# Performance work log

Hardware: AMD Instinct MI355X
Metric: run time of the kernel (lower is better)

Reference implementation:

```python
import jax, jax.numpy as jnp
import numpy as np

B, C, H, W = 4, 64, 64, 64
C2 = 2 * C
CR = C2 // 16  # SE bottleneck

def setup_inputs() -> dict:
    key = jax.random.key(0)
    ks = jax.random.split(key, 8)
    stdv = 1.0 / np.sqrt(C)
    return {
        "x1": jax.random.normal(ks[0], (B, C, H, W), jnp.float32),
        "x2": jax.random.normal(ks[1], (B, C, H, W), jnp.float32),
        "weight": jax.random.uniform(ks[2], (C, C), jnp.float32, -stdv, stdv),
        "weight2": jax.random.uniform(ks[3], (C, C), jnp.float32, -stdv, stdv),
        "ca_fc1": jax.random.normal(ks[4], (CR, C2), jnp.float32) * 0.05,  # 1x1 conv as matrix
        "ca_fc2": jax.random.normal(ks[5], (C2, CR), jnp.float32) * 0.05,
        "conv_w": jax.random.normal(ks[6], (C, C2), jnp.float32) * 0.05,  # 1x1 conv 2C->C
        "conv_b": jnp.zeros((C,), jnp.float32),
    }

def reference(x1, x2, weight, weight2, ca_fc1, ca_fc2, conv_w, conv_b):
    b, c, h, w = x2.shape
    n = h * w
    a1 = x1.reshape(b, c, n)  # x1 flattened [B,C,N]
    a2 = x2.reshape(b, c, n)  # x2 flattened [B,C,N]
    # Non-local branch: f = theta_x @ phi_x = a1^T @ a2 -> [B,N,N]
    f = jnp.einsum('bcn,bcm->bnm', a1, a2)
    adj = jax.nn.softmax(f, axis=-1)
    support = jnp.einsum('bcn,cd->bnd', a2, weight)  # g_x @ W, [B,N,C]
    y = jnp.einsum('bnm,bmd->bnd', adj, support)     # adj @ support
    y = y.transpose(0, 2, 1).reshape(b, c, h, w)
    # Channel-affinity branch: c_x = a_x @ b_x -> [B,C,C]
    c_x = jnp.einsum('bcn,bdn->bcd', a1, a2)
    support2 = jnp.einsum('bcd,de->bce', c_x, weight2)   # [B,C,C]
    y2 = jnp.einsum('bcd,bdn->bcn', support2, a1).reshape(b, c, h, w)
    z = jnp.concatenate([y, y2], axis=1)  # [B,2C,H,W]
    # ChannelAttention: global max pool -> fc1 -> relu -> fc2 -> sigmoid
    mp = jnp.max(z, axis=(2, 3))                       # [B,2C]
    hdn = jax.nn.relu(jnp.einsum('be,re->br', mp, ca_fc1))
    v = jax.nn.sigmoid(jnp.einsum('br,er->be', hdn, ca_fc2))  # [B,2C]
    out = z * v[:, :, None, None] + z
    out = jnp.einsum('behw,oe->bohw', out, conv_w) + conv_b[None, :, None, None]
    return out
```

## Files before the change

### kernel.cpp

```cpp
#include <hip/hip_runtime.h>
#include <hip/hip_bf16.h>
#include <math.h>

#define B_   4
#define C_   64
#define N_   4096
#define C2_  128

using frag  = __attribute__((ext_vector_type(8))) short;
using f32x4 = __attribute__((ext_vector_type(4))) float;
using f4    = __attribute__((ext_vector_type(4))) float;

__device__ __forceinline__ unsigned short f2bf(float f) {
  unsigned int u = __float_as_uint(f);
  u += 0x7fffu + ((u >> 16) & 1u);
  return (unsigned short)(u >> 16);
}
__device__ __forceinline__ float bf2f(unsigned short h) {
  return __uint_as_float(((unsigned int)h) << 16);
}
__device__ __forceinline__ unsigned int pkbf(float a, float b) {
  __hip_bfloat16 ha = __float2bfloat16(a), hb = __float2bfloat16(b);
  unsigned short ua, ub;
  __builtin_memcpy(&ua, &ha, 2);
  __builtin_memcpy(&ub, &hb, 2);
  return (unsigned int)ua | ((unsigned int)ub << 16);
}
__device__ __forceinline__ frag pk8(f4 lo, f4 hi) {
  frag f;
  unsigned int* u = (unsigned int*)&f;
  u[0] = pkbf(lo.x, lo.y);
  u[1] = pkbf(lo.z, lo.w);
  u[2] = pkbf(hi.x, hi.y);
  u[3] = pkbf(hi.z, hi.w);
  return f;
}
__device__ __forceinline__ f4 max4(f4 a, f4 b) {
  return (f4){fmaxf(a.x, b.x), fmaxf(a.y, b.y), fmaxf(a.z, b.z), fmaxf(a.w, b.w)};
}

__global__ __launch_bounds__(256) void prep_kernel(const float* __restrict__ x1,
                                                   const float* __restrict__ x2,
                                                   unsigned short* __restrict__ a1t,
                                                   unsigned short* __restrict__ a2t) {
  __shared__ float tA[64 * 33];
  __shared__ float tB[64 * 33];
  int b = blockIdx.y, n0 = blockIdx.x * 32, tid = threadIdx.x;
  {
    int n = tid & 31, cq = tid >> 5;
#pragma unroll
    for (int k = 0; k < 8; ++k) {
      int c = cq + 8 * k;
      tA[c * 33 + n] = x2[((size_t)(b * C_ + c)) * N_ + n0 + n];
      tB[c * 33 + n] = x1[((size_t)(b * C_ + c)) * N_ + n0 + n];
    }
  }
  __syncthreads();
  {
    int c = tid & 63, nq = tid >> 6;
#pragma unroll
    for (int k = 0; k < 8; ++k) {
      int n2 = nq + 4 * k;
      a2t[((size_t)b * N_ + n0 + n2) * C_ + c] = f2bf(tA[c * 33 + n2]);
      a1t[((size_t)b * N_ + n0 + n2) * C_ + c] = f2bf(tB[c * 33 + n2]);
    }
  }
}

__global__ __launch_bounds__(256) void support_mm_kernel(const float* __restrict__ weight,
                                                         const unsigned short* __restrict__ a2t,
                                                         unsigned short* __restrict__ vT) {
  __shared__ float Wl[64 * 65];
  int b = blockIdx.y, n0 = blockIdx.x * 32, tid = threadIdx.x;
  int wave = tid >> 6, lane = tid & 63, l16 = lane & 15, lq = lane >> 4;
#pragma unroll
  for (int k = 0; k < 16; ++k) {
    int lin = tid + 256 * k;
    Wl[(lin >> 6) * 65 + (lin & 63)] = weight[lin];
  }
  frag b0[2], b1[2];
#pragma unroll
  for (int ng = 0; ng < 2; ++ng) {
    const unsigned short* bp = a2t + ((size_t)b * N_ + n0 + ng * 16 + l16) * C_;
    b0[ng] = *(const frag*)(bp + lq * 8);
    b1[ng] = *(const frag*)(bp + 32 + lq * 8);
  }
  __syncthreads();
  int dd = 16 * wave + l16;
  frag aw[2];
#pragma unroll
  for (int ks = 0; ks < 2; ++ks) {
    float wv[8];
#pragma unroll
    for (int j = 0; j < 8; ++j) wv[j] = Wl[(ks * 32 + lq * 8 + j) * 65 + dd];
    aw[ks] = pk8((f4){wv[0], wv[1], wv[2], wv[3]}, (f4){wv[4], wv[5], wv[6], wv[7]});
  }
  f32x4 acc[2];
#pragma unroll
  for (int ng = 0; ng < 2; ++ng) {
    acc[ng] = (f32x4){0.f, 0.f, 0.f, 0.f};
    acc[ng] = __builtin_amdgcn_mfma_f32_16x16x32_bf16(aw[0], b0[ng], acc[ng], 0, 0, 0);
    acc[ng] = __builtin_amdgcn_mfma_f32_16x16x32_bf16(aw[1], b1[ng], acc[ng], 0, 0, 0);
  }
#pragma unroll
  for (int ng = 0; ng < 2; ++ng)
#pragma unroll
    for (int r = 0; r < 4; ++r)
      vT[((size_t)(b * C_) + 16 * wave + 4 * lq + r) * N_ + n0 + ng * 16 + l16] =
          f2bf(acc[ng][r]);
}

__global__ __launch_bounds__(256) void cxmm_kernel(const float* __restrict__ x1,
                                                   const float* __restrict__ x2,
                                                   float* __restrict__ cxp) {
  int b = blockIdx.y, seg = blockIdx.x, tid = threadIdx.x;
  int wave = tid >> 6, lane = tid & 63, l16 = lane & 15, lq = lane >> 4;
  int n0 = seg * 64;
  const float* a2r = x2 + ((size_t)(b * C_) + 16 * wave + l16) * N_ + n0 + lq * 8;
  frag afr[2];
#pragma unroll
  for (int ks = 0; ks < 2; ++ks)
    afr[ks] = pk8(*(const f4*)(a2r + ks * 32), *(const f4*)(a2r + ks * 32 + 4));
  f32x4 acc[4];
#pragma unroll
  for (int cg = 0; cg < 4; ++cg) acc[cg] = (f32x4){0.f, 0.f, 0.f, 0.f};
#pragma unroll
  for (int cg = 0; cg < 4; ++cg) {
    const float* a1r = x1 + ((size_t)(b * C_) + cg * 16 + l16) * N_ + n0 + lq * 8;
#pragma unroll
    for (int ks = 0; ks < 2; ++ks) {
      frag bfr = pk8(*(const f4*)(a1r + ks * 32), *(const f4*)(a1r + ks * 32 + 4));
      acc[cg] = __builtin_amdgcn_mfma_f32_16x16x32_bf16(afr[ks], bfr, acc[cg], 0, 0, 0);
    }
  }
  float* op = cxp + ((size_t)(b * 64 + seg)) * 4096;
#pragma unroll
  for (int cg = 0; cg < 4; ++cg)
#pragma unroll
    for (int r = 0; r < 4; ++r)
      op[(16 * wave + 4 * lq + r) * 64 + cg * 16 + l16] = acc[cg][r];
}

__global__ __launch_bounds__(256) void cxred_kernel(const float* __restrict__ cxp,
                                                    float* __restrict__ cx) {
  int idx = blockIdx.x * 256 + threadIdx.x;
  int b = idx >> 12, r = idx & 4095;
  const float* p = cxp + (size_t)b * 64 * 4096 + r;
  float s = 0.f;
#pragma unroll 8
  for (int sg = 0; sg < 64; ++sg) s += p[(size_t)sg * 4096];
  cx[idx] = s;
}

__global__ __launch_bounds__(256) void s2bf_kernel(const float* __restrict__ cx,
                                                   const float* __restrict__ w2,
                                                   unsigned short* __restrict__ s2bf) {
  __shared__ float cxl[4096];
  __shared__ float w2l[4096];
  int b = blockIdx.x, tid = threadIdx.x;
#pragma unroll
  for (int k = 0; k < 16; ++k) {
    int lin = tid + 256 * k;
    cxl[lin] = cx[(size_t)b * 4096 + lin];
    w2l[lin] = w2[lin];
  }
  __syncthreads();
  int c = tid & 63, eg = tid >> 6;
  float acc[16];
#pragma unroll
  for (int i = 0; i < 16; ++i) acc[i] = 0.f;
  for (int d = 0; d < 64; ++d) {
    float a = cxl[d * 64 + c];
#pragma unroll
    for (int i = 0; i < 16; ++i) acc[i] += a * w2l[d * 64 + eg * 16 + i];
  }
  unsigned short* op = s2bf + (size_t)b * 4096 + c * 64 + eg * 16;
#pragma unroll
  for (int i = 0; i < 8; ++i)
    *(unsigned int*)(op + 2 * i) = pkbf(acc[2 * i], acc[2 * i + 1]);
}

template <int SEG>
__global__ __launch_bounds__(256) void attn_kernel(const unsigned short* __restrict__ a1t,
                                                   const unsigned short* __restrict__ a2t,
                                                   const unsigned short* __restrict__ vT,
                                                   float* __restrict__ z,
                                                   unsigned short* __restrict__ Opart,
                                                   float* __restrict__ ml) {
  __shared__ unsigned short Kt[2][64 * 64];
  __shared__ unsigned short Vt[2][64 * 64];
  __shared__ uint2 Pl[4][16 * 16];

  const int b = blockIdx.y, n0 = blockIdx.x * 64, tid = threadIdx.x;
  const int seg = (SEG > 1) ? blockIdx.z : 0;
  const int wave = tid >> 6, lane = tid & 63;
  const int l16 = lane & 15, lq = lane >> 4;
  const int NT = N_ / SEG / 64;
  const int mbase = seg * (N_ / SEG);

  const unsigned short* qbase = a1t + ((size_t)b * N_ + n0 + wave * 16 + l16) * C_;
  frag qa0 = *(const frag*)(qbase + lq * 8);
  frag qa1 = *(const frag*)(qbase + 32 + lq * 8);

  f32x4 O[4];
#pragma unroll
  for (int i = 0; i < 4; ++i) O[i] = (f32x4){0.f, 0.f, 0.f, 0.f};
  float m_l = -1e30f, l_l = 0.f;

  const unsigned short* a2b = a2t + (size_t)b * N_ * C_;
  const unsigned short* vTb = vT + (size_t)b * C_ * N_;
  char* Pw = (char*)&Pl[wave][0];
  const int swzP = (l16 & 7) << 4;

  const int srow0 = tid >> 3, scb = tid & 7;
  const int srow1 = (tid + 256) >> 3;
  const int kswz0 = (scb * 16) ^ ((srow0 & 7) << 4);
  const int kswz1 = (scb * 16) ^ ((srow1 & 7) << 4);

  frag k0 = *(const frag*)(a2b + (size_t)(mbase + srow0) * C_ + scb * 8);
  frag k1 = *(const frag*)(a2b + (size_t)(mbase + srow1) * C_ + scb * 8);
  frag v0 = *(const frag*)(vTb + (size_t)srow0 * N_ + mbase + scb * 8);
  frag v1 = *(const frag*)(vTb + (size_t)srow1 * N_ + mbase + scb * 8);
  *(frag*)((char*)&Kt[0][0] + srow0 * 128 + kswz0) = k0;
  *(frag*)((char*)&Kt[0][0] + srow1 * 128 + kswz1) = k1;
  *(frag*)((char*)&Vt[0][0] + srow0 * 128 + kswz0) = v0;
  *(frag*)((char*)&Vt[0][0] + srow1 * 128 + kswz1) = v1;
  __syncthreads();

  int cur = 0;
  for (int t = 0; t < NT; ++t, cur ^= 1) {
    if (t + 1 < NT) {
      int mn = mbase + (t + 1) * 64;
      k0 = *(const frag*)(a2b + (size_t)(mn + srow0) * C_ + scb * 8);
      k1 = *(const frag*)(a2b + (size_t)(mn + srow1) * C_ + scb * 8);
      v0 = *(const frag*)(vTb + (size_t)srow0 * N_ + mn + scb * 8);
      v1 = *(const frag*)(vTb + (size_t)srow1 * N_ + mn + scb * 8);
    }

    f32x4 S[4];
    __builtin_amdgcn_s_setprio(1);
#pragma unroll
    for (int ms = 0; ms < 4; ++ms) {
      int m = ms * 16 + l16;
      int swz = (m & 7) << 4;
      frag kb0 = *(const frag*)((char*)&Kt[cur][0] + m * 128 + ((lq * 16) ^ swz));
      frag kb1 = *(const frag*)((char*)&Kt[cur][0] + m * 128 + ((64 + lq * 16) ^ swz));
      f32x4 acc = (f32x4){0.f, 0.f, 0.f, 0.f};
      acc = __builtin_amdgcn_mfma_f32_16x16x32_bf16(kb0, qa0, acc, 0, 0, 0);
      acc = __builtin_amdgcn_mfma_f32_16x16x32_bf16(kb1, qa1, acc, 0, 0, 0);
      S[ms] = acc;
    }
    __builtin_amdgcn_s_setprio(0);

    float mx0 = fmaxf(fmaxf(S[0][0], S[0][1]), fmaxf(S[0][2], S[0][3]));
    float mx1 = fmaxf(fmaxf(S[1][0], S[1][1]), fmaxf(S[1][2], S[1][3]));
    float mx2 = fmaxf(fmaxf(S[2][0], S[2][1]), fmaxf(S[2][2], S[2][3]));
    float mx3 = fmaxf(fmaxf(S[3][0], S[3][1]), fmaxf(S[3][2], S[3][3]));
    float mx = fmaxf(fmaxf(mx0, mx1), fmaxf(mx2, mx3));
    mx = fmaxf(mx, __shfl_xor(mx, 16, 64));
    mx = fmaxf(mx, __shfl_xor(mx, 32, 64));

    if (!__all(mx <= m_l + 8.f)) {
      float mn = fmaxf(m_l, mx);
      float sc = __expf(m_l - mn);
      m_l = mn;
      l_l *= sc;
      float scb_[4];
#pragma unroll
      for (int r = 0; r < 4; ++r) scb_[r] = __shfl(sc, 20 * lq + r, 64);
#pragma unroll
      for (int ds = 0; ds < 4; ++ds)
#pragma unroll
        for (int r = 0; r < 4; ++r) O[ds][r] *= scb_[r];
    }

    float p[16];
    float rs = 0.f;
#pragma unroll
    for (int ms = 0; ms < 4; ++ms)
#pragma unroll
      for (int r = 0; r < 4; ++r) {
        float e = __expf(S[ms][r] - m_l);
        p[ms * 4 + r] = e;
        rs += e;
      }
    rs += __shfl_xor(rs, 16, 64);
    rs += __shfl_xor(rs, 32, 64);
    l_l += rs;

#pragma unroll
    for (int ms = 0; ms < 4; ++ms) {
      uint2 w;
      w.x = pkbf(p[ms * 4 + 0], p[ms * 4 + 1]);
      w.y = pkbf(p[ms * 4 + 2], p[ms * 4 + 3]);
      *(uint2*)(Pw + l16 * 128 + ((32 * ms + 8 * lq) ^ swzP)) = w;
    }
    asm volatile("s_waitcnt lgkmcnt(0)" ::: "memory");
    __builtin_amdgcn_sched_barrier(0);

    frag pa0 = *(const frag*)(Pw + l16 * 128 + ((lq * 16) ^ swzP));
    frag pa1 = *(const frag*)(Pw + l16 * 128 + ((64 + lq * 16) ^ swzP));
    __builtin_amdgcn_s_setprio(1);
#pragma unroll
    for (int ds = 0; ds < 4; ++ds) {
      int d = ds * 16 + l16;
      int swz = (d & 7) << 4;
      frag vb0 = *(const frag*)((char*)&Vt[cur][0] + d * 128 + ((lq * 16) ^ swz));
      frag vb1 = *(const frag*)((char*)&Vt[cur][0] + d * 128 + ((64 + lq * 16) ^ swz));
      O[ds] = __builtin_amdgcn_mfma_f32_16x16x32_bf16(pa0, vb0, O[ds], 0, 0, 0);
      O[ds] = __builtin_amdgcn_mfma_f32_16x16x32_bf16(pa1, vb1, O[ds], 0, 0, 0);
    }
    __builtin_amdgcn_s_setprio(0);

    if (t + 1 < NT) {
      *(frag*)((char*)&Kt[cur ^ 1][0] + srow0 * 128 + kswz0) = k0;
      *(frag*)((char*)&Kt[cur ^ 1][0] + srow1 * 128 + kswz1) = k1;
      *(frag*)((char*)&Vt[cur ^ 1][0] + srow0 * 128 + kswz0) = v0;
      *(frag*)((char*)&Vt[cur ^ 1][0] + srow1 * 128 + kswz1) = v1;
      __syncthreads();
    }
  }

  if (SEG > 1) {
    size_t base = (size_t)(b * SEG + seg) * N_ + n0 + wave * 16;
    if (lq == 0) {
      ml[(base + l16) * 2]     = m_l;
      ml[(base + l16) * 2 + 1] = l_l;
    }
#pragma unroll
    for (int r = 0; r < 4; ++r)
#pragma unroll
      for (int ds = 0; ds < 4; ++ds)
        Opart[(base + lq * 4 + r) * 64 + ds * 16 + l16] = f2bf(O[ds][r]);
  } else {
    float inv[4];
#pragma unroll
    for (int r = 0; r < 4; ++r) inv[r] = 1.f / __shfl(l_l, 20 * lq + r, 64);
#pragma unroll
    for (int ds = 0; ds < 4; ++ds)
#pragma unroll
      for (int r = 0; r < 4; ++r)
        z[((size_t)b * N_ + n0 + wave * 16 + lq * 4 + r) * 128 + ds * 16 + l16] = O[ds][r] * inv[r];
  }
}

__global__ __launch_bounds__(256) void combine_kernel(const unsigned short* __restrict__ Opart,
                                                      const float* __restrict__ ml,
                                                      float* __restrict__ z,
                                                      float* __restrict__ mppA) {
  __shared__ float zsm[64][65];
  int b = blockIdx.y, tid = threadIdx.x;
  int nr = tid >> 2;
  int n = blockIdx.x * 64 + nr;
  int dq = (tid & 3) * 16;
  float mv[4], lv[4], M = -1e30f;
#pragma unroll
  for (int s = 0; s < 4; ++s) {
    size_t r = (size_t)(b * 4 + s) * N_ + n;
    mv[s] = ml[r * 2];
    lv[s] = ml[r * 2 + 1];
    M = fmaxf(M, mv[s]);
  }
  float acc[16];
#pragma unroll
  for (int j = 0; j < 16; ++j) acc[j] = 0.f;
  float l = 0.f;
#pragma unroll
  for (int s = 0; s < 4; ++s) {
    float w = __expf(mv[s] - M);
    l += w * lv[s];
    const unsigned short* op = Opart + ((size_t)(b * 4 + s) * N_ + n) * 64 + dq;
    frag p0 = *(const frag*)(op);
    frag p1 = *(const frag*)(op + 8);
#pragma unroll
    for (int j = 0; j < 8; ++j) {
      acc[j]     += w * bf2f((unsigned short)p0[j]);
      acc[8 + j] += w * bf2f((unsigned short)p1[j]);
    }
  }
  float inv = 1.f / l;
  float* zp = z + ((size_t)b * N_ + n) * 128 + dq;
#pragma unroll
  for (int k = 0; k < 4; ++k) {
    f4 res = (f4){acc[4 * k] * inv, acc[4 * k + 1] * inv,
                  acc[4 * k + 2] * inv, acc[4 * k + 3] * inv};
    *(f4*)(zp + k * 4) = res;
    zsm[nr][dq + 4 * k]     = res.x;
    zsm[nr][dq + 4 * k + 1] = res.y;
    zsm[nr][dq + 4 * k + 2] = res.z;
    zsm[nr][dq + 4 * k + 3] = res.w;
  }
  __syncthreads();
  if (tid < 64) {
    float mx = -1e30f;
    for (int nn = 0; nn < 64; ++nn) mx = fmaxf(mx, zsm[nn][tid]);
    mppA[((size_t)b * 64 + blockIdx.x) * 64 + tid] = mx;
  }
}

__global__ __launch_bounds__(256) void mpA_kernel(const float* __restrict__ z,
                                                  float* __restrict__ mppA) {
  __shared__ float red[4][64];
  int b = blockIdx.y, n0 = blockIdx.x * 64, tid = threadIdx.x;
  int e = tid & 63, g = tid >> 6;
  float mx = -1e30f;
#pragma unroll
  for (int k = 0; k < 16; ++k)
    mx = fmaxf(mx, z[((size_t)b * N_ + n0 + g + 4 * k) * 128 + e]);
  red[g][e] = mx;
  __syncthreads();
  if (tid < 64)
    mppA[((size_t)b * 64 + blockIdx.x) * 64 + tid] =
        fmaxf(fmaxf(red[0][tid], red[1][tid]), fmaxf(red[2][tid], red[3][tid]));
}

__global__ __launch_bounds__(256) void y2_kernel(const unsigned short* __restrict__ s2bf,
                                                 const unsigned short* __restrict__ a1t,
                                                 float* __restrict__ z,
                                                 float* __restrict__ mppB) {
  __shared__ f4 red[4][4][16];
  int b = blockIdx.y, n0 = blockIdx.x * 32, tid = threadIdx.x;
  int wave = tid >> 6, lane = tid & 63, l16 = lane & 15, lq = lane >> 4;
  const unsigned short* s2r = s2bf + (size_t)b * 4096 + (16 * wave + l16) * 64;
  frag sa0 = *(const frag*)(s2r + lq * 8);
  frag sa1 = *(const frag*)(s2r + 32 + lq * 8);
  f4 mx = (f4){-1e30f, -1e30f, -1e30f, -1e30f};
#pragma unroll
  for (int j = 0; j < 2; ++j) {
    const unsigned short* bp = a1t + ((size_t)b * N_ + n0 + 16 * j + l16) * 64;
    frag b0 = *(const frag*)(bp + lq * 8);
    frag b1 = *(const frag*)(bp + 32 + lq * 8);
    f32x4 acc = (f32x4){0.f, 0.f, 0.f, 0.f};
    acc = __builtin_amdgcn_mfma_f32_16x16x32_bf16(sa0, b0, acc, 0, 0, 0);
    acc = __builtin_amdgcn_mfma_f32_16x16x32_bf16(sa1, b1, acc, 0, 0, 0);
    *(f4*)(z + ((size_t)b * N_ + n0 + 16 * j + l16) * 128 + 64 + 16 * wave + 4 * lq) = acc;
#pragma unroll
    for (int r = 0; r < 4; ++r) mx[r] = fmaxf(mx[r], acc[r]);
  }
  red[wave][lq][l16] = mx;
  __syncthreads();
  if (tid < 64) {
    int w = tid >> 4, q = (tid >> 2) & 3, r = tid & 3;
    float m = -1e30f;
#pragma unroll
    for (int l = 0; l < 16; ++l) m = fmaxf(m, red[w][q][l][r]);
    mppB[((size_t)b * 128 + blockIdx.x) * 64 + 16 * w + 4 * q + r] = m;
  }
}

__global__ __launch_bounds__(256) void ca2_kernel(const float* __restrict__ mppA,
                                                  const float* __restrict__ mppB,
                                                  const float* __restrict__ fc1,
                                                  const float* __restrict__ fc2,
                                                  float* __restrict__ vbuf) {
  __shared__ f4 red4[256];
  __shared__ float mpl[128];
  __shared__ float red2[8][33];
  __shared__ float hl[8];
  int b = blockIdx.x, t = threadIdx.x;
  {
    const f4* src = (const f4*)(mppA + (size_t)b * 64 * 64);
    f4 m = src[t];
    m = max4(m, src[t + 256]);
    m = max4(m, src[t + 512]);
    m = max4(m, src[t + 768]);
    red4[t] = m;
  }
  __syncthreads();
  if (t < 16) {
    f4 m = red4[t];
#pragma unroll
    for (int j = 1; j < 16; ++j) m = max4(m, red4[t + 16 * j]);
    *(f4*)&mpl[t * 4] = m;
  }
  __syncthreads();
  {
    const f4* src = (const f4*)(mppB + (size_t)b * 128 * 64);
    f4 m = src[t];
#pragma unroll
    for (int k = 1; k < 8; ++k) m = max4(m, src[t + 256 * k]);
    red4[t] = m;
  }
  __syncthreads();
  if (t < 16) {
    f4 m = red4[t];
#pragma unroll
    for (int j = 1; j < 16; ++j) m = max4(m, red4[t + 16 * j]);
    *(f4*)&mpl[64 + t * 4] = m;
  }
  __syncthreads();
  {
    int r = t >> 5, j = t & 31;
    const f4 mv = *(const f4*)&mpl[j * 4];
    const f4 wv = *(const f4*)(fc1 + r * 128 + j * 4);
    red2[r][j] = mv.x * wv.x + mv.y * wv.y + mv.z * wv.z + mv.w * wv.w;
  }
  __syncthreads();
  if (t < 8) {
    float s = 0.f;
#pragma unroll
    for (int j = 0; j < 32; ++j) s += red2[t][j];
    hl[t] = fmaxf(s, 0.f);
  }
  __syncthreads();
  if (t < 128) {
    float s = 0.f;
    const float* f2r = fc2 + t * 8;
#pragma unroll
    for (int r = 0; r < 8; ++r) s += hl[r] * f2r[r];
    vbuf[b * 128 + t] = 1.f + 1.f / (1.f + __expf(-s));
  }
}

__global__ __launch_bounds__(256) void conv_kernel(const float* __restrict__ z,
                                                   const float* __restrict__ vbuf,
                                                   const float* __restrict__ conv_w,
                                                   const float* __restrict__ conv_b,
                                                   float* __restrict__ out) {
  __shared__ unsigned short zv[64 * 128];
  int b = blockIdx.y, n0 = blockIdx.x * 64, tid = threadIdx.x;
  int wave = tid >> 6, lane = tid & 63, l16 = lane & 15, lq = lane >> 4;
  {
    int e4 = tid & 31;
    f4 vq = *(const f4*)(vbuf + b * 128 + e4 * 4);
#pragma unroll
    for (int k = 0; k < 8; ++k) {
      int row = (tid >> 5) + 8 * k;
      f4 zq = *(const f4*)(z + ((size_t)(b * N_) + n0 + row) * 128 + e4 * 4);
      zq *= vq;
      uint2 w;
      w.x = pkbf(zq.x, zq.y);
      w.y = pkbf(zq.z, zq.w);
      *(uint2*)((char*)zv + row * 256 + ((e4 * 8) ^ ((row & 7) << 4))) = w;
    }
  }
  const float* cwr = conv_w + (size_t)(16 * wave + l16) * 128 + lq * 8;
  frag aw[4];
#pragma unroll
  for (int ks = 0; ks < 4; ++ks)
    aw[ks] = pk8(*(const f4*)(cwr + ks * 32), *(const f4*)(cwr + ks * 32 + 4));
  __syncthreads();
  f32x4 acc[4];
#pragma unroll
  for (int ng = 0; ng < 4; ++ng) acc[ng] = (f32x4){0.f, 0.f, 0.f, 0.f};
#pragma unroll
  for (int ng = 0; ng < 4; ++ng) {
    int n = ng * 16 + l16;
    int swz = (n & 7) << 4;
#pragma unroll
    for (int ks = 0; ks < 4; ++ks) {
      frag bz = *(const frag*)((char*)zv + n * 256 + ((ks * 64 + lq * 16) ^ swz));
      acc[ng] = __builtin_amdgcn_mfma_f32_16x16x32_bf16(aw[ks], bz, acc[ng], 0, 0, 0);
    }
  }
#pragma unroll
  for (int r = 0; r < 4; ++r) {
    int o = 16 * wave + 4 * lq + r;
    float bias = conv_b[o];
#pragma unroll
    for (int ng = 0; ng < 4; ++ng)
      out[((size_t)(b * C_ + o)) * N_ + n0 + ng * 16 + l16] = acc[ng][r] + bias;
  }
}

extern "C" void kernel_launch(void* const* d_in, const int* in_sizes, int n_in,
                              void* d_out, int out_size, void* d_ws, size_t ws_size,
                              hipStream_t stream) {
  const float* x1      = (const float*)d_in[0];
  const float* x2      = (const float*)d_in[1];
  const float* weight  = (const float*)d_in[2];
  const float* weight2 = (const float*)d_in[3];
  const float* fc1     = (const float*)d_in[4];
  const float* fc2     = (const float*)d_in[5];
  const float* conv_w  = (const float*)d_in[6];
  const float* conv_b  = (const float*)d_in[7];
  float* out = (float*)d_out;

  char* ws = (char*)d_ws;
  unsigned short* a1t = (unsigned short*)(ws + 0);
  unsigned short* a2t = (unsigned short*)(ws + 2097152);
  float* mppA = (float*)(ws + 2097152);
  float* mppB = (float*)(ws + 2162688);
  unsigned short* s2bf = (unsigned short*)(ws + 2293760);
  unsigned short* vT  = (unsigned short*)(ws + 4194304);
  float* z    = (float*)(ws + 6291456);
  float* cxp  = (float*)(ws + 6291456);
  float* cx   = (float*)(ws + 14680064);
  float* vbuf = (float*)(ws + 14745600);
  unsigned short* Opart = (unsigned short*)(ws + 14764544);
  float* ml   = (float*)(ws + 23153152);
  const bool seg4 = ws_size >= 23677440ull;

  cxmm_kernel<<<dim3(64, 4), 256, 0, stream>>>(x1, x2, cxp);
  prep_kernel<<<dim3(128, 4), 256, 0, stream>>>(x1, x2, a1t, a2t);
  support_mm_kernel<<<dim3(128, 4), 256, 0, stream>>>(weight, a2t, vT);
  cxred_kernel<<<dim3(64), 256, 0, stream>>>(cxp, cx);
  if (seg4) {
    attn_kernel<4><<<dim3(64, 4, 4), 256, 0, stream>>>(a1t, a2t, vT, z, Opart, ml);
    combine_kernel<<<dim3(64, 4), 256, 0, stream>>>(Opart, ml, z, mppA);
  } else {
    attn_kernel<1><<<dim3(64, 4), 256, 0, stream>>>(a1t, a2t, vT, z, nullptr, nullptr);
    mpA_kernel<<<dim3(64, 4), 256, 0, stream>>>(z, mppA);
  }
  s2bf_kernel<<<dim3(4), 256, 0, stream>>>(cx, weight2, s2bf);
  y2_kernel<<<dim3(128, 4), 256, 0, stream>>>(s2bf, a1t, z, mppB);
  ca2_kernel<<<dim3(4), 256, 0, stream>>>(mppA, mppB, fc1, fc2, vbuf);
  conv_kernel<<<dim3(64, 4), 256, 0, stream>>>(z, vbuf, conv_w, conv_b, out);
}
```

Baseline: 81.83 us.

## Fuse channel-affinity matmul into prep and widen attention blocks to 512 threads

The separate cxmm kernel is removed and its partial c_x product is computed inside prep_kernel, reusing the x1/x2 tiles already staged in shared memory, so one launch and a second global read of the inputs disappear. prep now handles 64 columns per block. The attention kernel runs 8 waves per block covering 128 query rows, so each K/V tile loaded into LDS is shared by twice as many queries and each thread stages one fragment instead of two. This halves the attention grid, which may reduce occupancy or latency hiding, and raises per-block LDS and register pressure.

```diff
diff --git a/kernel.cpp b/kernel.cpp
--- a/kernel.cpp
+++ b/kernel.cpp
@@ -42,28 +42,62 @@
 __global__ __launch_bounds__(256) void prep_kernel(const float* __restrict__ x1,
                                                    const float* __restrict__ x2,
                                                    unsigned short* __restrict__ a1t,
-                                                   unsigned short* __restrict__ a2t) {
-  __shared__ float tA[64 * 33];
-  __shared__ float tB[64 * 33];
-  int b = blockIdx.y, n0 = blockIdx.x * 32, tid = threadIdx.x;
+                                                   unsigned short* __restrict__ a2t,
+                                                   float* __restrict__ cxp) {
+  __shared__ float tA[64 * 65];
+  __shared__ float tB[64 * 65];
+  int b = blockIdx.y, n0 = blockIdx.x * 64, tid = threadIdx.x;
+  int wave = tid >> 6, lane = tid & 63, l16 = lane & 15, lq = lane >> 4;
   {
-    int n = tid & 31, cq = tid >> 5;
-#pragma unroll
-    for (int k = 0; k < 8; ++k) {
-      int c = cq + 8 * k;
-      tA[c * 33 + n] = x2[((size_t)(b * C_ + c)) * N_ + n0 + n];
-      tB[c * 33 + n] = x1[((size_t)(b * C_ + c)) * N_ + n0 + n];
+    int n = tid & 63, cq = tid >> 6;
+#pragma unroll
+    for (int k = 0; k < 16; ++k) {
+      int c = cq + 4 * k;
+      tA[c * 65 + n] = x2[((size_t)(b * C_ + c)) * N_ + n0 + n];
+      tB[c * 65 + n] = x1[((size_t)(b * C_ + c)) * N_ + n0 + n];
     }
   }
   __syncthreads();
   {
     int c = tid & 63, nq = tid >> 6;
 #pragma unroll
-    for (int k = 0; k < 8; ++k) {
+    for (int k = 0; k < 16; ++k) {
       int n2 = nq + 4 * k;
-      a2t[((size_t)b * N_ + n0 + n2) * C_ + c] = f2bf(tA[c * 33 + n2]);
-      a1t[((size_t)b * N_ + n0 + n2) * C_ + c] = f2bf(tB[c * 33 + n2]);
-    }
+      a2t[((size_t)b * N_ + n0 + n2) * C_ + c] = f2bf(tA[c * 65 + n2]);
+      a1t[((size_t)b * N_ + n0 + n2) * C_ + c] = f2bf(tB[c * 65 + n2]);
+    }
+  }
+  {
+    int dd = 16 * wave + l16;
+    frag afr[2];
+#pragma unroll
+    for (int ks = 0; ks < 2; ++ks) {
+      float w0[8];
+#pragma unroll
+      for (int j = 0; j < 8; ++j) w0[j] = tA[dd * 65 + ks * 32 + lq * 8 + j];
+      afr[ks] = pk8((f4){w0[0], w0[1], w0[2], w0[3]}, (f4){w0[4], w0[5], w0[6], w0[7]});
+    }
+    f32x4 acc[4];
+#pragma unroll
+    for (int cg = 0; cg < 4; ++cg) acc[cg] = (f32x4){0.f, 0.f, 0.f, 0.f};
+#pragma unroll
+    for (int cg = 0; cg < 4; ++cg) {
+      int cc = cg * 16 + l16;
+#pragma unroll
+      for (int ks = 0; ks < 2; ++ks) {
+        float w0[8];
+#pragma unroll
+        for (int j = 0; j < 8; ++j) w0[j] = tB[cc * 65 + ks * 32 + lq * 8 + j];
+        frag bfr = pk8((f4){w0[0], w0[1], w0[2], w0[3]}, (f4){w0[4], w0[5], w0[6], w0[7]});
+        acc[cg] = __builtin_amdgcn_mfma_f32_16x16x32_bf16(afr[ks], bfr, acc[cg], 0, 0, 0);
+      }
+    }
+    float* op = cxp + ((size_t)(b * 64 + blockIdx.x)) * 4096;
+#pragma unroll
+    for (int cg = 0; cg < 4; ++cg)
+#pragma unroll
+      for (int r = 0; r < 4; ++r)
+        op[(16 * wave + 4 * lq + r) * 64 + cg * 16 + l16] = acc[cg][r];
   }
 }
 
@@ -108,37 +142,6 @@
     for (int r = 0; r < 4; ++r)
       vT[((size_t)(b * C_) + 16 * wave + 4 * lq + r) * N_ + n0 + ng * 16 + l16] =
           f2bf(acc[ng][r]);
-}
-
-__global__ __launch_bounds__(256) void cxmm_kernel(const float* __restrict__ x1,
-                                                   const float* __restrict__ x2,
-                                                   float* __restrict__ cxp) {
-  int b = blockIdx.y, seg = blockIdx.x, tid = threadIdx.x;
-  int wave = tid >> 6, lane = tid & 63, l16 = lane & 15, lq = lane >> 4;
-  int n0 = seg * 64;
-  const float* a2r = x2 + ((size_t)(b * C_) + 16 * wave + l16) * N_ + n0 + lq * 8;
-  frag afr[2];
-#pragma unroll
-  for (int ks = 0; ks < 2; ++ks)
-    afr[ks] = pk8(*(const f4*)(a2r + ks * 32), *(const f4*)(a2r + ks * 32 + 4));
-  f32x4 acc[4];
-#pragma unroll
-  for (int cg = 0; cg < 4; ++cg) acc[cg] = (f32x4){0.f, 0.f, 0.f, 0.f};
-#pragma unroll
-  for (int cg = 0; cg < 4; ++cg) {
-    const float* a1r = x1 + ((size_t)(b * C_) + cg * 16 + l16) * N_ + n0 + lq * 8;
-#pragma unroll
-    for (int ks = 0; ks < 2; ++ks) {
-      frag bfr = pk8(*(const f4*)(a1r + ks * 32), *(const f4*)(a1r + ks * 32 + 4));
-      acc[cg] = __builtin_amdgcn_mfma_f32_16x16x32_bf16(afr[ks], bfr, acc[cg], 0, 0, 0);
-    }
-  }
-  float* op = cxp + ((size_t)(b * 64 + seg)) * 4096;
-#pragma unroll
-  for (int cg = 0; cg < 4; ++cg)
-#pragma unroll
-    for (int r = 0; r < 4; ++r)
-      op[(16 * wave + 4 * lq + r) * 64 + cg * 16 + l16] = acc[cg][r];
 }
 
 __global__ __launch_bounds__(256) void cxred_kernel(const float* __restrict__ cxp,
@@ -181,7 +184,7 @@
 }
 
 template <int SEG>
-__global__ __launch_bounds__(256) void attn_kernel(const unsigned short* __restrict__ a1t,
+__global__ __launch_bounds__(512) void attn_kernel(const unsigned short* __restrict__ a1t,
                                                    const unsigned short* __restrict__ a2t,
                                                    const unsigned short* __restrict__ vT,
                                                    float* __restrict__ z,
@@ -189,9 +192,9 @@
                                                    float* __restrict__ ml) {
   __shared__ unsigned short Kt[2][64 * 64];
   __shared__ unsigned short Vt[2][64 * 64];
-  __shared__ uint2 Pl[4][16 * 16];
-
-  const int b = blockIdx.y, n0 = blockIdx.x * 64, tid = threadIdx.x;
+  __shared__ uint2 Pl[8][16 * 16];
+
+  const int b = blockIdx.y, n0 = blockIdx.x * 128, tid = threadIdx.x;
   const int seg = (SEG > 1) ? blockIdx.z : 0;
   const int wave = tid >> 6, lane = tid & 63;
   const int l16 = lane & 15, lq = lane >> 4;
@@ -212,29 +215,21 @@
   char* Pw = (char*)&Pl[wave][0];
   const int swzP = (l16 & 7) << 4;
 
-  const int srow0 = tid >> 3, scb = tid & 7;
-  const int srow1 = (tid + 256) >> 3;
-  const int kswz0 = (scb * 16) ^ ((srow0 & 7) << 4);
-  const int kswz1 = (scb * 16) ^ ((srow1 & 7) << 4);
-
-  frag k0 = *(const frag*)(a2b + (size_t)(mbase + srow0) * C_ + scb * 8);
-  frag k1 = *(const frag*)(a2b + (size_t)(mbase + srow1) * C_ + scb * 8);
-  frag v0 = *(const frag*)(vTb + (size_t)srow0 * N_ + mbase + scb * 8);
-  frag v1 = *(const frag*)(vTb + (size_t)srow1 * N_ + mbase + scb * 8);
-  *(frag*)((char*)&Kt[0][0] + srow0 * 128 + kswz0) = k0;
-  *(frag*)((char*)&Kt[0][0] + srow1 * 128 + kswz1) = k1;
-  *(frag*)((char*)&Vt[0][0] + srow0 * 128 + kswz0) = v0;
-  *(frag*)((char*)&Vt[0][0] + srow1 * 128 + kswz1) = v1;
+  const int srow = tid >> 3, scb = tid & 7;
+  const int kswz = (scb * 16) ^ ((srow & 7) << 4);
+
+  frag k0 = *(const frag*)(a2b + (size_t)(mbase + srow) * C_ + scb * 8);
+  frag v0 = *(const frag*)(vTb + (size_t)srow * N_ + mbase + scb * 8);
+  *(frag*)((char*)&Kt[0][0] + srow * 128 + kswz) = k0;
+  *(frag*)((char*)&Vt[0][0] + srow * 128 + kswz) = v0;
   __syncthreads();
 
   int cur = 0;
   for (int t = 0; t < NT; ++t, cur ^= 1) {
     if (t + 1 < NT) {
       int mn = mbase + (t + 1) * 64;
-      k0 = *(const frag*)(a2b + (size_t)(mn + srow0) * C_ + scb * 8);
-      k1 = *(const frag*)(a2b + (size_t)(mn + srow1) * C_ + scb * 8);
-      v0 = *(const frag*)(vTb + (size_t)srow0 * N_ + mn + scb * 8);
-      v1 = *(const frag*)(vTb + (size_t)srow1 * N_ + mn + scb * 8);
+      k0 = *(const frag*)(a2b + (size_t)(mn + srow) * C_ + scb * 8);
+      v0 = *(const frag*)(vTb + (size_t)srow * N_ + mn + scb * 8);
     }
 
     f32x4 S[4];
@@ -313,10 +308,8 @@
     __builtin_amdgcn_s_setprio(0);
 
     if (t + 1 < NT) {
-      *(frag*)((char*)&Kt[cur ^ 1][0] + srow0 * 128 + kswz0) = k0;
-      *(frag*)((char*)&Kt[cur ^ 1][0] + srow1 * 128 + kswz1) = k1;
-      *(frag*)((char*)&Vt[cur ^ 1][0] + srow0 * 128 + kswz0) = v0;
-      *(frag*)((char*)&Vt[cur ^ 1][0] + srow1 * 128 + kswz1) = v1;
+      *(frag*)((char*)&Kt[cur ^ 1][0] + srow * 128 + kswz) = k0;
+      *(frag*)((char*)&Vt[cur ^ 1][0] + srow * 128 + kswz) = v0;
       __syncthreads();
     }
   }
@@ -591,15 +584,14 @@
   float* ml   = (float*)(ws + 23153152);
   const bool seg4 = ws_size >= 23677440ull;
 
-  cxmm_kernel<<<dim3(64, 4), 256, 0, stream>>>(x1, x2, cxp);
-  prep_kernel<<<dim3(128, 4), 256, 0, stream>>>(x1, x2, a1t, a2t);
+  prep_kernel<<<dim3(64, 4), 256, 0, stream>>>(x1, x2, a1t, a2t, cxp);
   support_mm_kernel<<<dim3(128, 4), 256, 0, stream>>>(weight, a2t, vT);
   cxred_kernel<<<dim3(64), 256, 0, stream>>>(cxp, cx);
   if (seg4) {
-    attn_kernel<4><<<dim3(64, 4, 4), 256, 0, stream>>>(a1t, a2t, vT, z, Opart, ml);
+    attn_kernel<4><<<dim3(32, 4, 4), 512, 0, stream>>>(a1t, a2t, vT, z, Opart, ml);
     combine_kernel<<<dim3(64, 4), 256, 0, stream>>>(Opart, ml, z, mppA);
   } else {
-    attn_kernel<1><<<dim3(64, 4), 256, 0, stream>>>(a1t, a2t, vT, z, nullptr, nullptr);
+    attn_kernel<1><<<dim3(32, 4), 512, 0, stream>>>(a1t, a2t, vT, z, nullptr, nullptr);
     mpA_kernel<<<dim3(64, 4), 256, 0, stream>>>(z, mppA);
   }
   s2bf_kernel<<<dim3(4), 256, 0, stream>>>(cx, weight2, s2bf);
```

After: 74.59 us. -8.9%, faster.
